# Performance work log

Measured on AMD Instinct MI355X. Metric: run time of the kernel, lower is better.

## Reference

```python
import jax, jax.numpy as jnp
import numpy as np

TEMP = 1.0
BETA = 0.5
ALPHA = 0.5
GAMMA = 0.5


def _pairwise_sqdist(x, y):
    # squared euclidean distances [N, M]; clamp tiny negatives from cancellation
    xx = jnp.sum(x * x, axis=-1)
    yy = jnp.sum(y * y, axis=-1)
    d = xx[:, None] + yy[None, :] - 2.0 * (x @ y.T)
    return jnp.maximum(d, 0.0)


def setup_inputs() -> dict:
    key = jax.random.key(0)
    features = jax.random.normal(key, (16384, 128), dtype=jnp.float32)
    return {"features": features}


def reference(features):
    B = features.shape[0] // 2
    a = features[:B]
    b = features[B:]
    t2 = TEMP * TEMP

    # Positive term: only the diagonal of sim_ab is used, so compute it directly.
    # sim = 1 / ((temperature * cdist)^2 + 1) = 1 / (t^2 * sqdist + 1)
    pos_sq = jnp.sum((a - b) ** 2, axis=-1)              # [B]
    pos_sim = 1.0 / (t2 * pos_sq + 1.0)
    positive_loss = jnp.mean((pos_sim - 10.0) ** 2 - 2.0 * ALPHA * pos_sim)

    eye = jnp.eye(B, dtype=bool)

    def _neg(x):
        sim = 1.0 / (t2 * _pairwise_sqdist(x, x) + 1.0)   # [B, B]
        sim = jnp.where(eye, 0.0, sim)                     # zero the diagonal
        neg_loss = jnp.mean(jnp.sum(jnp.exp(BETA * sim) * sim, axis=-1))
        return neg_loss, jnp.sum(sim)

    nl_a, s_a = _neg(a)
    nl_b, s_b = _neg(b)

    negative_loss = nl_a + nl_b
    regularization = GAMMA * (s_a + s_b)
    return positive_loss + negative_loss + regularization
```

## Files before the change

### kernel.cpp

```cpp
#include <hip/hip_runtime.h>
#include <hip/hip_bf16.h>


typedef __attribute__((ext_vector_type(8))) short short8;
typedef __attribute__((ext_vector_type(4))) float float4v;

#define NROWS 16384
#define BHALF 8192
#define D 128
#define NT 64
#define NPAIRS 2080
#define NACC 64

__device__ __forceinline__ unsigned short f2bf(float x) {
    unsigned int u = __float_as_uint(x);
    u += 0x7fffu + ((u >> 16) & 1u);
    return (unsigned short)(u >> 16);
}

__global__ __launch_bounds__(256)
void prep_pos_kernel(const float* __restrict__ f,
                     unsigned short* __restrict__ xbf,
                     float* __restrict__ xx,
                     float* __restrict__ acc) {
    __shared__ float red[4];
    const int wave = threadIdx.x >> 6, lane = threadIdx.x & 63;
    const int gw = blockIdx.x * 4 + wave;
    float posAcc = 0.0f;

    #pragma unroll
    for (int p = 0; p < 16; ++p) {
        const int i = gw + p * 512;
        const float2 a = *reinterpret_cast<const float2*>(f + (size_t)i * D + lane * 2);
        const float2 b = *reinterpret_cast<const float2*>(f + (size_t)(i + BHALF) * D + lane * 2);
        ushort2 sa2, sb2;
        sa2.x = f2bf(a.x); sa2.y = f2bf(a.y);
        sb2.x = f2bf(b.x); sb2.y = f2bf(b.y);
        *reinterpret_cast<ushort2*>(xbf + (size_t)i * D + lane * 2) = sa2;
        *reinterpret_cast<ushort2*>(xbf + (size_t)(i + BHALF) * D + lane * 2) = sb2;
        float sa = a.x * a.x + a.y * a.y;
        float sb = b.x * b.x + b.y * b.y;
        float dx = a.x - b.x, dy = a.y - b.y;
        float sp = dx * dx + dy * dy;
        #pragma unroll
        for (int off = 32; off; off >>= 1) {
            sa += __shfl_down(sa, off, 64);
            sb += __shfl_down(sb, off, 64);
            sp += __shfl_down(sp, off, 64);
        }
        if (lane == 0) {
            xx[i] = sa;
            xx[i + BHALF] = sb;
            float ps = 1.0f / (sp + 1.0f);
            posAcc += (ps - 10.0f) * (ps - 10.0f) - ps;
        }
    }
    if (lane == 0) red[wave] = posAcc;
    __syncthreads();
    if (threadIdx.x == 0) {
        float s = (red[0] + red[1] + red[2] + red[3]) * (1.0f / (float)BHALF);
        atomicAdd(&acc[blockIdx.x & (NACC - 1)], s);
    }
}

__global__ __launch_bounds__(512, 4)
void neg_kernel(const unsigned short* __restrict__ xbf,
                const float* __restrict__ xx,
                float* __restrict__ acc) {
    __shared__ unsigned short lT[2][128 * 128];
    __shared__ float red[16];

    const int t = threadIdx.x;
    const int mat = blockIdx.y;
    const int moff = mat * BHALF;

    int rem = blockIdx.x, bi = 0;
    while (rem >= NT - bi) { rem -= NT - bi; ++bi; }
    const int tbi = bi, tbj = bi + rem;

    const int wave = t >> 6, lane = t & 63;

    #pragma unroll
    for (int half = 0; half < 2; ++half) {
        const int rowbase = moff + (half ? tbj : tbi) * 128;
        const char* gbase = (const char*)(xbf + (size_t)rowbase * D);
        #pragma unroll
        for (int p = 0; p < 4; ++p) {
            const int c = p * 512 + t;
            const int row = c >> 4, col16 = c & 15;
            const int gb = row * 256 + ((col16 * 16) ^ ((row & 7) << 4));
            const unsigned ldsoff = (unsigned)(p * 512 + wave * 64) * 16;
            __builtin_amdgcn_global_load_lds(
                (const __attribute__((address_space(1))) unsigned int*)(gbase + gb),
                (__attribute__((address_space(3))) unsigned int*)((char*)lT[half] + ldsoff),
                16, 0, 0);
        }
    }
    __syncthreads();

    const int wr = wave >> 1, wc = wave & 1;
    const int l15 = lane & 15, g = lane >> 4;

    float4v accv[2][4] = {};

    #pragma unroll
    for (int kk = 0; kk < 4; ++kk) {
        short8 a[2], b[4];
        #pragma unroll
        for (int mi = 0; mi < 2; ++mi) {
            const int row = wr * 32 + mi * 16 + l15;
            const int boff = (kk * 64 + g * 16) ^ ((row & 7) << 4);
            a[mi] = *reinterpret_cast<short8*>(reinterpret_cast<char*>(lT[0]) + row * 256 + boff);
        }
        #pragma unroll
        for (int ni = 0; ni < 4; ++ni) {
            const int row = wc * 64 + ni * 16 + l15;
            const int boff = (kk * 64 + g * 16) ^ ((row & 7) << 4);
            b[ni] = *reinterpret_cast<short8*>(reinterpret_cast<char*>(lT[1]) + row * 256 + boff);
        }
        #pragma unroll
        for (int mi = 0; mi < 2; ++mi)
            #pragma unroll
            for (int ni = 0; ni < 4; ++ni)
                accv[mi][ni] = __builtin_amdgcn_mfma_f32_16x16x32_bf16(a[mi], b[ni], accv[mi][ni], 0, 0, 0);
    }

    const bool diag = (tbi == tbj);
    const int rbase = tbi * 128 + wr * 32;
    const int cbase = tbj * 128 + wc * 64;

    float xr[8], xc[4];
    #pragma unroll
    for (int mi = 0; mi < 2; ++mi)
        #pragma unroll
        for (int r = 0; r < 4; ++r)
            xr[mi * 4 + r] = xx[moff + rbase + mi * 16 + g * 4 + r];
    #pragma unroll
    for (int ni = 0; ni < 4; ++ni)
        xc[ni] = xx[moff + cbase + ni * 16 + l15];

    float aS = 0.0f, aN = 0.0f;
    #pragma unroll
    for (int mi = 0; mi < 2; ++mi) {
        #pragma unroll
        for (int ni = 0; ni < 4; ++ni) {
            #pragma unroll
            for (int r = 0; r < 4; ++r) {
                const float dot = accv[mi][ni][r];
                float d = fmaxf(xr[mi * 4 + r] + xc[ni] - 2.0f * dot, 0.0f);
                float s = __builtin_amdgcn_rcpf(d + 1.0f);
                if (diag) {
                    const int row = rbase + mi * 16 + g * 4 + r;
                    const int col = cbase + ni * 16 + l15;
                    if (row == col) s = 0.0f;
                }
                aS += s;
                aN += __expf(0.5f * s) * s;
            }
        }
    }

    #pragma unroll
    for (int off = 32; off; off >>= 1) {
        aS += __shfl_down(aS, off, 64);
        aN += __shfl_down(aN, off, 64);
    }
    if (lane == 0) { red[wave * 2] = aS; red[wave * 2 + 1] = aN; }
    __syncthreads();
    if (t == 0) {
        float S = 0.0f, N = 0.0f;
        #pragma unroll
        for (int w = 0; w < 8; ++w) { S += red[w * 2]; N += red[w * 2 + 1]; }
        const float w = diag ? 1.0f : 2.0f;
        atomicAdd(&acc[(blockIdx.x * 2 + blockIdx.y) & (NACC - 1)],
                  w * (N * (1.0f / (float)BHALF) + 0.5f * S));
    }
}

__global__ void finish_kernel(const float* __restrict__ acc, float* __restrict__ out) {
    const int lane = threadIdx.x & 63;
    float v = acc[lane];
    #pragma unroll
    for (int off = 32; off; off >>= 1) v += __shfl_down(v, off, 64);
    if (lane == 0) out[0] = v;
}

extern "C" void kernel_launch(void* const* d_in, const int* in_sizes, int n_in,
                              void* d_out, int out_size, void* d_ws, size_t ws_size,
                              hipStream_t stream) {
    const float* f = (const float*)d_in[0];
    float* out = (float*)d_out;
    unsigned short* xbf = (unsigned short*)d_ws;
    float* xx = (float*)((char*)d_ws + (size_t)NROWS * D * sizeof(unsigned short));
    float* acc = xx + NROWS;

    hipMemsetAsync(acc, 0, NACC * sizeof(float), stream);
    prep_pos_kernel<<<128, 256, 0, stream>>>(f, xbf, xx, acc);
    neg_kernel<<<dim3(NPAIRS, 2), 512, 0, stream>>>(xbf, xx, acc);
    finish_kernel<<<1, 64, 0, stream>>>(acc, out);
}
```

Before: 117.7 us.

## Replace exp with cubic polynomial, drop memset, widen prep kernel grid

Several changes land together. The exp(0.5*s)*s term in the negative-pair epilogue becomes a cubic Taylor polynomial in s, and the distance-plus-one computation is folded into one fma followed by a max against 1. The accumulators are split in two to shorten dependency chains. The hipMemsetAsync is removed: the prep kernel now zeroes the accumulator and writes per-block partial sums instead of using atomics, and it runs 256 blocks of 512 threads instead of 128 of 256. The polynomial approximates exp over s in [0,1] with small truncation error, which changes numerics slightly.

Measured after the change: 104.9 us. 10.8% less time.

```diff
diff --git a/kernel.cpp b/kernel.cpp
--- a/kernel.cpp
+++ b/kernel.cpp
@@ -11,6 +11,7 @@
 #define NT 64
 #define NPAIRS 2080
 #define NACC 64
+#define NPART 256
 
 __device__ __forceinline__ unsigned short f2bf(float x) {
     unsigned int u = __float_as_uint(x);
@@ -18,19 +19,20 @@
     return (unsigned short)(u >> 16);
 }
 
-__global__ __launch_bounds__(256)
+__global__ __launch_bounds__(512)
 void prep_pos_kernel(const float* __restrict__ f,
                      unsigned short* __restrict__ xbf,
                      float* __restrict__ xx,
-                     float* __restrict__ acc) {
-    __shared__ float red[4];
+                     float* __restrict__ part,
+                     float* __restrict__ negacc) {
+    __shared__ float red[8];
     const int wave = threadIdx.x >> 6, lane = threadIdx.x & 63;
-    const int gw = blockIdx.x * 4 + wave;
+    const int gw = blockIdx.x * 8 + wave;
     float posAcc = 0.0f;
 
     #pragma unroll
-    for (int p = 0; p < 16; ++p) {
-        const int i = gw + p * 512;
+    for (int p = 0; p < 4; ++p) {
+        const int i = gw + p * 2048;
         const float2 a = *reinterpret_cast<const float2*>(f + (size_t)i * D + lane * 2);
         const float2 b = *reinterpret_cast<const float2*>(f + (size_t)(i + BHALF) * D + lane * 2);
         ushort2 sa2, sb2;
@@ -56,17 +58,20 @@
         }
     }
     if (lane == 0) red[wave] = posAcc;
+    if (blockIdx.x == 0 && threadIdx.x < NACC) negacc[threadIdx.x] = 0.0f;
     __syncthreads();
     if (threadIdx.x == 0) {
-        float s = (red[0] + red[1] + red[2] + red[3]) * (1.0f / (float)BHALF);
-        atomicAdd(&acc[blockIdx.x & (NACC - 1)], s);
+        float s = 0.0f;
+        #pragma unroll
+        for (int w = 0; w < 8; ++w) s += red[w];
+        part[blockIdx.x] = s;
     }
 }
 
 __global__ __launch_bounds__(512, 4)
 void neg_kernel(const unsigned short* __restrict__ xbf,
                 const float* __restrict__ xx,
-                float* __restrict__ acc) {
+                float* __restrict__ negacc) {
     __shared__ unsigned short lT[2][128 * 128];
     __shared__ float red[16];
 
@@ -129,17 +134,17 @@
     const int rbase = tbi * 128 + wr * 32;
     const int cbase = tbj * 128 + wc * 64;
 
-    float xr[8], xc[4];
+    float xr1[8], xc[4];
     #pragma unroll
     for (int mi = 0; mi < 2; ++mi)
         #pragma unroll
         for (int r = 0; r < 4; ++r)
-            xr[mi * 4 + r] = xx[moff + rbase + mi * 16 + g * 4 + r];
+            xr1[mi * 4 + r] = xx[moff + rbase + mi * 16 + g * 4 + r] + 1.0f;
     #pragma unroll
     for (int ni = 0; ni < 4; ++ni)
         xc[ni] = xx[moff + cbase + ni * 16 + l15];
 
-    float aS = 0.0f, aN = 0.0f;
+    float aS0 = 0.0f, aS1 = 0.0f, aN0 = 0.0f, aN1 = 0.0f;
     #pragma unroll
     for (int mi = 0; mi < 2; ++mi) {
         #pragma unroll
@@ -147,18 +152,23 @@
             #pragma unroll
             for (int r = 0; r < 4; ++r) {
                 const float dot = accv[mi][ni][r];
-                float d = fmaxf(xr[mi * 4 + r] + xc[ni] - 2.0f * dot, 0.0f);
-                float s = __builtin_amdgcn_rcpf(d + 1.0f);
+                float t1 = xr1[mi * 4 + r] + xc[ni];
+                float m = fmaxf(fmaf(dot, -2.0f, t1), 1.0f);
+                float s = __builtin_amdgcn_rcpf(m);
                 if (diag) {
                     const int row = rbase + mi * 16 + g * 4 + r;
                     const int col = cbase + ni * 16 + l15;
                     if (row == col) s = 0.0f;
                 }
-                aS += s;
-                aN += __expf(0.5f * s) * s;
+                float p = fmaf(s, 0.02083333333f, 0.125f);
+                p = fmaf(s, p, 0.5f);
+                p = fmaf(s, p, 1.0f);
+                if (r & 1) { aS1 += s; aN1 = fmaf(p, s, aN1); }
+                else       { aS0 += s; aN0 = fmaf(p, s, aN0); }
             }
         }
     }
+    float aS = aS0 + aS1, aN = aN0 + aN1;
 
     #pragma unroll
     for (int off = 32; off; off >>= 1) {
@@ -172,14 +182,18 @@
         #pragma unroll
         for (int w = 0; w < 8; ++w) { S += red[w * 2]; N += red[w * 2 + 1]; }
         const float w = diag ? 1.0f : 2.0f;
-        atomicAdd(&acc[(blockIdx.x * 2 + blockIdx.y) & (NACC - 1)],
+        atomicAdd(&negacc[(blockIdx.x * 2 + blockIdx.y) & (NACC - 1)],
                   w * (N * (1.0f / (float)BHALF) + 0.5f * S));
     }
 }
 
-__global__ void finish_kernel(const float* __restrict__ acc, float* __restrict__ out) {
+__global__ void finish_kernel(const float* __restrict__ negacc,
+                              const float* __restrict__ part,
+                              float* __restrict__ out) {
     const int lane = threadIdx.x & 63;
-    float v = acc[lane];
+    float v = negacc[lane];
+    float pp = part[lane] + part[lane + 64] + part[lane + 128] + part[lane + 192];
+    v = fmaf(pp, 1.0f / (float)BHALF, v);
     #pragma unroll
     for (int off = 32; off; off >>= 1) v += __shfl_down(v, off, 64);
     if (lane == 0) out[0] = v;
@@ -192,10 +206,10 @@
     float* out = (float*)d_out;
     unsigned short* xbf = (unsigned short*)d_ws;
     float* xx = (float*)((char*)d_ws + (size_t)NROWS * D * sizeof(unsigned short));
-    float* acc = xx + NROWS;
-
-    hipMemsetAsync(acc, 0, NACC * sizeof(float), stream);
-    prep_pos_kernel<<<128, 256, 0, stream>>>(f, xbf, xx, acc);
-    neg_kernel<<<dim3(NPAIRS, 2), 512, 0, stream>>>(xbf, xx, acc);
-    finish_kernel<<<1, 64, 0, stream>>>(acc, out);
-}
+    float* negacc = xx + NROWS;
+    float* part = negacc + NACC;
+
+    prep_pos_kernel<<<NPART, 512, 0, stream>>>(f, xbf, xx, part, negacc);
+    neg_kernel<<<dim3(NPAIRS, 2), 512, 0, stream>>>(xbf, xx, negacc);
+    finish_kernel<<<1, 64, 0, stream>>>(negacc, part, out);
+}
```
